# Optimization experiments

Measured on AMD Instinct MI355X. Metric: run time of the kernel, lower is better.

Reference implementation:

```python
import jax, jax.numpy as jnp
import numpy as np

N = 8192      # input_dim (graph nodes)
H = 256       # hidden_dim
KN = 128      # kernel_num
B = 2048      # batch size
W = 2 * H + 2 # conv kernel width


def setup_inputs() -> dict:
    key = jax.random.key(0)
    ks = jax.random.split(key, 10)
    a = float(np.sqrt(6.0 / (N + H)))  # xavier_uniform bound
    embedding = jax.random.uniform(ks[0], (N, H), minval=-a, maxval=a, dtype=jnp.float32)
    A = jax.random.normal(ks[1], (N, N), dtype=jnp.float32) * 0.01  # dense adjacency
    k1 = jax.random.normal(ks[2], (KN, 1, 1, W), dtype=jnp.float32) * 0.05  # filter_size=1
    b1 = jax.random.normal(ks[3], (KN,), dtype=jnp.float32) * 0.05
    k2 = jax.random.normal(ks[4], (KN, 1, 2, W), dtype=jnp.float32) * 0.05  # filter_size=2
    b2 = jax.random.normal(ks[5], (KN,), dtype=jnp.float32) * 0.05
    dense_w = jax.random.normal(ks[6], (2, KN * 4), dtype=jnp.float32) * 0.02
    dense_b = jax.random.normal(ks[7], (2,), dtype=jnp.float32) * 0.02
    batch_x = jax.random.randint(ks[8], (B,), 0, N)
    batch_y = jax.random.randint(ks[9], (B,), 0, N)
    return {"embedding": embedding, "A": A, "k1": k1, "b1": b1, "k2": k2,
            "b2": b2, "dense_w": dense_w, "dense_b": dense_b,
            "batch_x": batch_x, "batch_y": batch_y}


def _encode(t, kern, bias):
    # t: [B,1,1,2H]; Conv2d padding=1 both dims, kernel (f, 2H+2) -> out [B,KN,4-f,1]
    out = jax.lax.conv_general_dilated(
        t, kern, window_strides=(1, 1), padding=((1, 1), (1, 1)),
        dimension_numbers=("NCHW", "OIHW", "NCHW"))
    out = jax.nn.relu(out + bias[None, :, None, None])
    return jnp.max(out, axis=(2, 3))  # max_pool2d over full height, width==1 -> [B,KN]


def reference(embedding, A, k1, b1, k2, b2, dense_w, dense_b, batch_x, batch_y):
    # GCN layer (featureless): layer1 = A @ embedding, shape [N,H]
    layer1 = jnp.matmul(A, embedding)
    # Record path (the only path feeding the output): rQ=layer1[bx], rA=layer1[by];
    # ErQ = rA, ErA = rQ per the torch soft_attention record bookkeeping.
    rQ = layer1[batch_x]  # [B,H]
    rA = layer1[batch_y]  # [B,H]
    d = rQ - rA
    tq = d * d            # (rQ-ErQ)^2 == (rA-ErA)^2, symmetric
    mul = rQ * rA         # rQ*ErQ == rA*ErA
    t = jnp.concatenate([tq, mul], axis=1)[:, None, None, :]  # [B,1,1,2H]
    enc = jnp.concatenate([_encode(t, k1, b1), _encode(t, k2, b2)], axis=1)  # [B,2*KN]
    q_re = jax.nn.relu(enc)  # dropout is identity in eval mode
    a_re = q_re              # a-side computation is algebraically identical (symmetry above)
    re = jnp.concatenate([q_re, a_re], axis=1)  # [B,4*KN]
    score = jnp.matmul(re, dense_w.T) + dense_b  # [B,2]
    return jax.nn.log_softmax(score, axis=1)
```

## Files before the change

### kernel.cpp

```cpp
#include <hip/hip_runtime.h>
#include <stdint.h>
#include <math.h>

#define NN 8192
#define HD 256
#define BATCH 2048
#define KSPLIT 8
#define KCH (NN / KSPLIT)

typedef __attribute__((ext_vector_type(8))) short bf16x8;
typedef __attribute__((ext_vector_type(4))) float f32x4;

static __device__ __forceinline__ uint32_t pack_bf2(float x, float y) {
  union { float f; uint32_t u; } a, b; a.f = x; b.f = y;
  uint32_t ua = a.u + 0x7FFFu + ((a.u >> 16) & 1u);
  uint32_t ub = b.u + 0x7FFFu + ((b.u >> 16) & 1u);
  return (ua >> 16) | (ub & 0xFFFF0000u);
}
static __device__ __forceinline__ float bf_lo(uint32_t u) {
  return __uint_as_float(u << 16);
}
static __device__ __forceinline__ float bf_hi(uint32_t u) {
  return __uint_as_float(u & 0xFFFF0000u);
}

extern "C" __global__ void k_prep(const float* __restrict__ emb,
                                  const float* __restrict__ k1,
                                  const float* __restrict__ k2,
                                  uint16_t* __restrict__ Bm,
                                  uint16_t* __restrict__ Wm) {
  const int tid = threadIdx.x;
  if (blockIdx.x < 256) {
    __shared__ float ts[32][257];
    const int kc = blockIdx.x;
#pragma unroll
    for (int i = 0; i < 32; i++)
      ts[i][tid] = emb[(size_t)(kc * 32 + i) * HD + tid];
    __syncthreads();
#pragma unroll
    for (int c = 0; c < 4; c++) {
      int e = c * 256 + tid;
      int ci = e >> 6, l = e & 63;
      int g = l >> 4, col = ci * 16 + (l & 15);
      uint4 v;
      v.x = pack_bf2(ts[g * 8 + 0][col], ts[g * 8 + 1][col]);
      v.y = pack_bf2(ts[g * 8 + 2][col], ts[g * 8 + 3][col]);
      v.z = pack_bf2(ts[g * 8 + 4][col], ts[g * 8 + 5][col]);
      v.w = pack_bf2(ts[g * 8 + 6][col], ts[g * 8 + 7][col]);
      ((uint4*)Bm)[(size_t)kc * 1024 + e] = v;
    }
  } else {
    const int c = (blockIdx.x - 256) * 256 + tid;
    const int lcl = c & 63;
    const int ci = (c >> 6) % 24;
    const int kc = c / (24 * 64);
    const int j = ci * 16 + (lcl & 15);
    const int k0 = kc * 32 + ((lcl >> 4) << 3);
    float f[8];
#pragma unroll
    for (int jj = 0; jj < 8; jj++) {
      int k = k0 + jj;
      f[jj] = (j < 128) ? k1[j * 514 + 1 + k]
            : (j < 256) ? k2[(j - 128) * 1028 + 515 + k]
                        : k2[(j - 256) * 1028 + 1 + k];
    }
    uint4 v;
    v.x = pack_bf2(f[0], f[1]); v.y = pack_bf2(f[2], f[3]);
    v.z = pack_bf2(f[4], f[5]); v.w = pack_bf2(f[6], f[7]);
    *(uint4*)(Wm + (size_t)c * 8) = v;
  }
}

extern "C" __global__ __launch_bounds__(256, 2)
void k_gemm(const float* __restrict__ A, const uint16_t* __restrict__ Bm,
            const int* __restrict__ bx, const int* __restrict__ by,
            uint16_t* __restrict__ Rp) {
  __shared__ __align__(16) uint16_t Asm[64 * 512];
  const int tid = threadIdx.x;
  const int kblk = blockIdx.x & 7;
  const int mblk = blockIdx.x >> 3;
  const int wv = tid >> 6, l = tid & 63, g = l >> 4, l15 = l & 15;

  const int r = tid >> 2, b = tid & 3;
  const int gr = mblk * 64 + r;
  const int arow = (gr < BATCH) ? bx[gr] : by[gr - BATCH];
  const float* aSrc = A + (size_t)arow * NN + (size_t)kblk * KCH + b * 4;
  const int ris = r >> 4, l15s = r & 15;
  const int joff = (b & 1) << 2;
  const int gb = b >> 1;

#define PACK1(v_, m_) { \
    const int kcp = (m_) >> 1; \
    const int gg = (((m_) & 1) << 1) + gb; \
    const int off = ((kcp * 4 + ris) * 64 + gg * 16 + l15s) * 8 + joff; \
    uint2 u_; u_.x = pack_bf2((v_).x, (v_).y); u_.y = pack_bf2((v_).z, (v_).w); \
    *(uint2*)(Asm + off) = u_; }

#pragma unroll
  for (int half = 0; half < 2; ++half) {
    float4 t[16];
#pragma unroll
    for (int m16 = 0; m16 < 16; ++m16)
      t[m16] = *(const float4*)(aSrc + (half * 16 + m16) * 16);
#pragma unroll
    for (int m16 = 0; m16 < 16; ++m16) PACK1(t[m16], half * 16 + m16);
  }
  __syncthreads();

  f32x4 acc[4][4] = {};
  const uint16_t* bWave = Bm + (((size_t)(kblk * 32) * 16 + wv * 4) * 64 + l) * 8;

#define COMPUTE_RANGE(stage, kc0, kc1) \
  _Pragma("unroll") \
  for (int kc = (kc0); kc < (kc1); ++kc) { \
    bf16x8 bfr[4]; \
    _Pragma("unroll") \
    for (int cj = 0; cj < 4; ++cj) \
      bfr[cj] = *(const bf16x8*)(bWave + (((stage) * 16 + kc) * 16 + cj) * 512); \
    _Pragma("unroll") \
    for (int ri = 0; ri < 4; ++ri) { \
      bf16x8 af = *(const bf16x8*)(Asm + (size_t)((kc * 4 + ri) * 64 + l) * 8); \
      _Pragma("unroll") \
      for (int cj = 0; cj < 4; ++cj) \
        acc[ri][cj] = __builtin_amdgcn_mfma_f32_16x16x32_bf16( \
            af, bfr[cj], acc[ri][cj], 0, 0, 0); } }

  float4 s2a[16];
#pragma unroll
  for (int m = 0; m < 16; ++m)
    s2a[m] = *(const float4*)(aSrc + 512 + m * 16);
  COMPUTE_RANGE(0, 0, 8)
  float4 s2b[16];
#pragma unroll
  for (int m = 0; m < 16; ++m)
    s2b[m] = *(const float4*)(aSrc + 512 + (16 + m) * 16);
  COMPUTE_RANGE(0, 8, 16)
  __syncthreads();
#pragma unroll
  for (int m = 0; m < 16; ++m) PACK1(s2a[m], m)
#pragma unroll
  for (int m = 0; m < 16; ++m) PACK1(s2b[m], 16 + m)
  __syncthreads();
  COMPUTE_RANGE(1, 0, 16)
  __syncthreads();

  uint16_t* Ct = Asm;
#pragma unroll
  for (int ri = 0; ri < 4; ri++)
#pragma unroll
    for (int cj = 0; cj < 4; cj++)
#pragma unroll
      for (int rr = 0; rr < 4; rr++) {
        float v = acc[ri][cj][rr];
        float vn = __shfl_xor(v, 1);
        if ((l15 & 1) == 0) {
          int row16 = ri * 16 + g * 4 + rr;
          int col = wv * 64 + cj * 16 + l15;
          *(uint32_t*)(Ct + row16 * 256 + col) = pack_bf2(v, vn);
        }
      }
  __syncthreads();
  {
    const int row2 = tid >> 2, cb = (tid & 3) * 64;
    const uint4* src = (const uint4*)(Ct + row2 * 256 + cb);
    uint16_t* dst = Rp + ((size_t)kblk * 4096 + mblk * 64 + row2) * HD + cb;
    uint4 v0 = src[0], v1 = src[1], v2 = src[2], v3 = src[3];
    ((uint4*)dst)[0] = v0; ((uint4*)dst)[1] = v1;
    ((uint4*)dst)[2] = v2; ((uint4*)dst)[3] = v3;
  }
#undef PACK1
#undef COMPUTE_RANGE
}

extern "C" __global__ __launch_bounds__(256, 2)
void k_tail(const uint16_t* __restrict__ Rp, const uint16_t* __restrict__ Wm,
            const float* __restrict__ b1, const float* __restrict__ b2,
            const float* __restrict__ dw, const float* __restrict__ dbias,
            float* __restrict__ out) {
  __shared__ __align__(16) uint16_t t_frag[16 * 64 * 8];
  __shared__ float Cl[8][388];
  __shared__ float coef[6][128];
  const int tid = threadIdx.x;
  const int b0 = blockIdx.x * 8;
  const int wv = tid >> 6, l = tid & 63, g = l >> 4, l15 = l & 15;
  if (tid < 128) {
    coef[0][tid] = dw[tid] + dw[256 + tid];
    coef[1][tid] = dw[128 + tid] + dw[384 + tid];
    coef[2][tid] = dw[512 + tid] + dw[768 + tid];
    coef[3][tid] = dw[640 + tid] + dw[896 + tid];
    coef[4][tid] = b1[tid];
    coef[5][tid] = b2[tid];
  }
  {
    const int r = tid >> 5, c8 = (tid & 31) * 8;
    float rq[8] = {}, ra[8] = {};
#pragma unroll
    for (int p = 0; p < KSPLIT; p++) {
      uint4 q4 = *(const uint4*)(Rp + ((size_t)p * 4096 + b0 + r) * HD + c8);
      uint4 a4 = *(const uint4*)(Rp + ((size_t)p * 4096 + BATCH + b0 + r) * HD + c8);
      const uint32_t* qw = (const uint32_t*)&q4;
      const uint32_t* aw = (const uint32_t*)&a4;
#pragma unroll
      for (int w = 0; w < 4; w++) {
        rq[2 * w] += bf_lo(qw[w]); rq[2 * w + 1] += bf_hi(qw[w]);
        ra[2 * w] += bf_lo(aw[w]); ra[2 * w + 1] += bf_hi(aw[w]);
      }
    }
    uint32_t tq[4], ml[4];
#pragma unroll
    for (int w = 0; w < 4; w++) {
      float d0 = rq[2 * w] - ra[2 * w], d1 = rq[2 * w + 1] - ra[2 * w + 1];
      tq[w] = pack_bf2(d0 * d0, d1 * d1);
      ml[w] = pack_bf2(rq[2 * w] * ra[2 * w], rq[2 * w + 1] * ra[2 * w + 1]);
    }
    const int kc1 = c8 >> 5, gm = (c8 >> 3) & 3;
    const int kc2 = 8 + kc1;
    *(uint4*)(t_frag + (kc1 * 64 + gm * 16 + r) * 8) = *(uint4*)tq;
    *(uint4*)(t_frag + (kc2 * 64 + gm * 16 + r) * 8) = *(uint4*)ml;
    uint4 z = {0, 0, 0, 0};
    *(uint4*)(t_frag + (kc1 * 64 + gm * 16 + 8 + r) * 8) = z;
    *(uint4*)(t_frag + (kc2 * 64 + gm * 16 + 8 + r) * 8) = z;
  }
  __syncthreads();
  {
    f32x4 acc[6] = {};
    const uint16_t* wB = Wm + ((size_t)(wv * 6) * 64 + l) * 8;
#pragma unroll 2
    for (int kc = 0; kc < 16; kc++) {
      bf16x8 af = *(const bf16x8*)(t_frag + (kc * 64 + l) * 8);
#pragma unroll
      for (int ci = 0; ci < 6; ci++) {
        bf16x8 w = *(const bf16x8*)(wB + (size_t)kc * 12288 + ci * 512);
        acc[ci] = __builtin_amdgcn_mfma_f32_16x16x32_bf16(af, w, acc[ci], 0, 0, 0);
      }
    }
#pragma unroll
    for (int ci = 0; ci < 6; ci++)
#pragma unroll
      for (int rr = 0; rr < 4; rr++) {
        int row16 = g * 4 + rr;
        if (row16 < 8) Cl[row16][wv * 96 + ci * 16 + l15] = acc[ci][rr];
      }
  }
  __syncthreads();
  {
    const int r = tid >> 5, ch0 = (tid & 31) * 4;
    float s0 = 0.f, s1 = 0.f;
#pragma unroll
    for (int cc = 0; cc < 4; cc++) {
      const int c = ch0 + cc;
      float d1 = Cl[r][c], d2a = Cl[r][128 + c], d2b = Cl[r][256 + c];
      float bb1 = coef[4][c], bb2 = coef[5][c];
      float e1 = fmaxf(0.f, fmaxf(bb1, d1 + bb1));
      float e2 = fmaxf(0.f, fmaxf(d2a + bb2, d2b + bb2));
      s0 += e1 * coef[0][c] + e2 * coef[1][c];
      s1 += e1 * coef[2][c] + e2 * coef[3][c];
    }
#pragma unroll
    for (int off = 16; off >= 1; off >>= 1) {
      s0 += __shfl_xor(s0, off, 32);
      s1 += __shfl_xor(s1, off, 32);
    }
    if ((tid & 31) == 0) {
      s0 += dbias[0]; s1 += dbias[1];
      float m = fmaxf(s0, s1);
      float lse = m + logf(expf(s0 - m) + expf(s1 - m));
      out[(b0 + r) * 2] = s0 - lse;
      out[(b0 + r) * 2 + 1] = s1 - lse;
    }
  }
}

extern "C" void kernel_launch(void* const* d_in, const int* in_sizes, int n_in,
                              void* d_out, int out_size, void* d_ws, size_t ws_size,
                              hipStream_t stream) {
  const float* emb = (const float*)d_in[0];
  const float* A   = (const float*)d_in[1];
  const float* k1  = (const float*)d_in[2];
  const float* b1  = (const float*)d_in[3];
  const float* k2  = (const float*)d_in[4];
  const float* b2  = (const float*)d_in[5];
  const float* dw  = (const float*)d_in[6];
  const float* dbi = (const float*)d_in[7];
  const int* bx = (const int*)d_in[8];
  const int* by = (const int*)d_in[9];
  float* out = (float*)d_out;
  char* ws = (char*)d_ws;
  uint16_t* Bm = (uint16_t*)ws;
  uint16_t* Wm = (uint16_t*)(ws + (4u << 20));
  uint16_t* Rp = (uint16_t*)(ws + (8u << 20));

  k_prep<<<352, 256, 0, stream>>>(emb, k1, k2, Bm, Wm);
  k_gemm<<<64 * KSPLIT, 256, 0, stream>>>(A, Bm, bx, by, Rp);
  k_tail<<<256, 256, 0, stream>>>(Rp, Wm, b1, b2, dw, dbi, out);
}
```

Baseline: 61.23 us.

## Deduplicate gathered adjacency rows before GEMM and remap them in the tail

```diff
diff --git a/kernel.cpp b/kernel.cpp
--- a/kernel.cpp
+++ b/kernel.cpp
@@ -71,19 +71,90 @@
   }
 }
 
+extern "C" __global__ __launch_bounds__(1024)
+void k_dedup(const int* __restrict__ bx, const int* __restrict__ by,
+             int* __restrict__ uidx, int* __restrict__ ulist,
+             int* __restrict__ nuOut) {
+  __shared__ int table[NN];
+  __shared__ int rows[4096];
+  __shared__ int wsum[32];
+  const int tid = threadIdx.x;
+#pragma unroll
+  for (int k = 0; k < 8; ++k) table[tid + k * 1024] = 0x7fffffff;
+#pragma unroll
+  for (int k = 0; k < 4; ++k) {
+    const int i = tid + k * 1024;
+    rows[i] = (i < BATCH) ? bx[i] : by[i - BATCH];
+  }
+  __syncthreads();
+#pragma unroll
+  for (int k = 0; k < 4; ++k) {
+    const int i = tid + k * 1024;
+    atomicMin(&table[rows[i]], i);
+  }
+  __syncthreads();
+  const int base = tid * 4;
+  int f[4], s = 0;
+#pragma unroll
+  for (int k = 0; k < 4; ++k) {
+    const int i = base + k;
+    f[k] = (table[rows[i]] == i) ? 1 : 0;
+    s += f[k];
+  }
+  const int lane = tid & 63, wid = tid >> 6;
+  int incl = s;
+#pragma unroll
+  for (int off = 1; off < 64; off <<= 1) {
+    int v = __shfl_up(incl, off);
+    if (lane >= off) incl += v;
+  }
+  const int excl = incl - s;
+  if (lane == 63) wsum[wid] = incl;
+  __syncthreads();
+  if (tid == 0) {
+    int acc = 0;
+    for (int w = 0; w < 16; ++w) { int v = wsum[w]; wsum[w] = acc; acc += v; }
+    wsum[16] = acc;
+    *nuOut = acc;
+  }
+  __syncthreads();
+  int sl = wsum[wid] + excl;
+  int myslot[4];
+#pragma unroll
+  for (int k = 0; k < 4; ++k) { myslot[k] = sl; sl += f[k]; }
+  __syncthreads();
+#pragma unroll
+  for (int k = 0; k < 4; ++k) {
+    const int i = base + k;
+    if (f[k]) {
+      table[rows[i]] = myslot[k];
+      ulist[myslot[k]] = rows[i];
+    }
+  }
+  __syncthreads();
+#pragma unroll
+  for (int k = 0; k < 4; ++k) {
+    const int i = base + k;
+    uidx[i] = table[rows[i]];
+  }
+  const int nu = wsum[16];
+  for (int i = tid; i < 4096; i += 1024)
+    if (i >= nu) ulist[i] = 0;
+}
+
 extern "C" __global__ __launch_bounds__(256, 2)
 void k_gemm(const float* __restrict__ A, const uint16_t* __restrict__ Bm,
-            const int* __restrict__ bx, const int* __restrict__ by,
+            const int* __restrict__ ulist, const int* __restrict__ nuP,
             uint16_t* __restrict__ Rp) {
+  const int kblk = blockIdx.x & 7;
+  const int mblk = blockIdx.x >> 3;
+  if (mblk * 64 >= *nuP) return;
   __shared__ __align__(16) uint16_t Asm[64 * 512];
   const int tid = threadIdx.x;
-  const int kblk = blockIdx.x & 7;
-  const int mblk = blockIdx.x >> 3;
   const int wv = tid >> 6, l = tid & 63, g = l >> 4, l15 = l & 15;
 
   const int r = tid >> 2, b = tid & 3;
-  const int gr = mblk * 64 + r;
-  const int arow = (gr < BATCH) ? bx[gr] : by[gr - BATCH];
+  const int arow = ulist[mblk * 64 + r];
   const float* aSrc = A + (size_t)arow * NN + (size_t)kblk * KCH + b * 4;
   const int ris = r >> 4, l15s = r & 15;
   const int joff = (b & 1) << 2;
@@ -174,6 +245,7 @@
 
 extern "C" __global__ __launch_bounds__(256, 2)
 void k_tail(const uint16_t* __restrict__ Rp, const uint16_t* __restrict__ Wm,
+            const int* __restrict__ uidx,
             const float* __restrict__ b1, const float* __restrict__ b2,
             const float* __restrict__ dw, const float* __restrict__ dbias,
             float* __restrict__ out) {
@@ -193,11 +265,13 @@
   }
   {
     const int r = tid >> 5, c8 = (tid & 31) * 8;
+    const int uq = uidx[b0 + r];
+    const int ua = uidx[BATCH + b0 + r];
     float rq[8] = {}, ra[8] = {};
 #pragma unroll
     for (int p = 0; p < KSPLIT; p++) {
-      uint4 q4 = *(const uint4*)(Rp + ((size_t)p * 4096 + b0 + r) * HD + c8);
-      uint4 a4 = *(const uint4*)(Rp + ((size_t)p * 4096 + BATCH + b0 + r) * HD + c8);
+      uint4 q4 = *(const uint4*)(Rp + ((size_t)p * 4096 + uq) * HD + c8);
+      uint4 a4 = *(const uint4*)(Rp + ((size_t)p * 4096 + ua) * HD + c8);
       const uint32_t* qw = (const uint32_t*)&q4;
       const uint32_t* aw = (const uint32_t*)&a4;
 #pragma unroll
@@ -289,8 +363,12 @@
   uint16_t* Bm = (uint16_t*)ws;
   uint16_t* Wm = (uint16_t*)(ws + (4u << 20));
   uint16_t* Rp = (uint16_t*)(ws + (8u << 20));
-
+  int* uidx  = (int*)(ws + (24u << 20));
+  int* ulist = (int*)(ws + (24u << 20) + (64u << 10));
+  int* nuP   = (int*)(ws + (24u << 20) + (128u << 10));
+
+  k_dedup<<<1, 1024, 0, stream>>>(bx, by, uidx, ulist, nuP);
   k_prep<<<352, 256, 0, stream>>>(emb, k1, k2, Bm, Wm);
-  k_gemm<<<64 * KSPLIT, 256, 0, stream>>>(A, Bm, bx, by, Rp);
-  k_tail<<<256, 256, 0, stream>>>(Rp, Wm, b1, b2, dw, dbi, out);
-}
+  k_gemm<<<64 * KSPLIT, 256, 0, stream>>>(A, Bm, ulist, nuP, Rp);
+  k_tail<<<BATCH / 8, 256, 0, stream>>>(Rp, Wm, uidx, b1, b2, dw, dbi, out);
+}
```

Result: slower. 62.78 us (+2.5%).
